# Kernel optimization log

Hardware: AMD Instinct MI355X
Metric: run time of the kernel (lower is better)

Reference implementation:

```python
import jax, jax.numpy as jnp
import numpy as np

B, C, H, W = 16, 512, 32, 32
GROUPS = 8
EPS = 1e-5


def setup_inputs() -> dict:
    key = jax.random.key(0)
    ks = jax.random.split(key, 7)
    s = 1.0 / np.sqrt(C)
    return {
        "x": jax.random.normal(ks[0], (B, C, H, W), dtype=jnp.float32),
        "gamma": jnp.ones((C,), dtype=jnp.float32),
        "beta": jnp.zeros((C,), dtype=jnp.float32),
        "w_qkv": jax.random.normal(ks[1], (3 * C, C), dtype=jnp.float32) * s,
        "b_qkv": jnp.zeros((3 * C,), dtype=jnp.float32),
        "w_proj": jax.random.normal(ks[2], (C, C), dtype=jnp.float32) * s,
        "b_proj": jnp.zeros((C,), dtype=jnp.float32),
    }


def group_norm(x, gamma, beta):
    b, c, h, w = x.shape
    xg = x.reshape(b, GROUPS, c // GROUPS, h, w)
    mean = xg.mean(axis=(2, 3, 4), keepdims=True)
    var = xg.var(axis=(2, 3, 4), keepdims=True)
    xn = ((xg - mean) * jax.lax.rsqrt(var + EPS)).reshape(b, c, h, w)
    return xn * gamma[None, :, None, None] + beta[None, :, None, None]


def reference(x, gamma, beta, w_qkv, b_qkv, w_proj, b_proj):
    b, c, h, w = x.shape
    n = h * w
    hn = group_norm(x, gamma, beta)
    # 1x1 conv == channel matmul: [3C, C] x [B, C, N] -> [B, 3C, N]
    qkv = jnp.einsum('oc,bcn->bon', w_qkv, hn.reshape(b, c, n)) + b_qkv[None, :, None]
    q, k, v = jnp.split(qkv, 3, axis=1)  # each [B, C, N]
    scale = c ** (-0.5)
    # scores [B, N, N]: q^T k
    attn = jax.nn.softmax(jnp.einsum('bcn,bcm->bnm', q, k) * scale, axis=-1)
    out = jnp.einsum('bnm,bcm->bcn', attn, v)  # [B, C, N]
    proj = jnp.einsum('oc,bcn->bon', w_proj, out) + b_proj[None, :, None]
    return x + proj.reshape(b, c, h, w)
```

## Files before the change

### kernel.cpp

```cpp
#include <hip/hip_runtime.h>


#define BATCH 16
#define CCH 512
#define NSP 1024
#define EPSV 1e-5f
#define BK 32
#define HT 4096

typedef short bf16x8 __attribute__((ext_vector_type(8)));
typedef float f32x4 __attribute__((ext_vector_type(4)));

__device__ __forceinline__ unsigned short f2bf(float f) {
    unsigned int u = __float_as_uint(f);
    u += 0x7FFF + ((u >> 16) & 1);
    return (unsigned short)(u >> 16);
}

__device__ __forceinline__ void glds16(const void* g, void* l) {
    __builtin_amdgcn_global_load_lds(
        (const __attribute__((address_space(1))) unsigned int*)g,
        (__attribute__((address_space(3))) unsigned int*)l, 16, 0, 0);
}

#define XCD_MAP(GX_LOG2, PER, xv, yv, bv)                 \
    const int lin_ = blockIdx.x;                          \
    const int xcd_ = lin_ & 7;                            \
    int slot_ = lin_ >> 3;                                \
    const int hi_ = (slot_ >= (PER)) ? 1 : 0;             \
    const int bv = xcd_ + 8 * hi_;                        \
    slot_ -= hi_ * (PER);                                 \
    const int xv = slot_ & ((1 << (GX_LOG2)) - 1);        \
    const int yv = slot_ >> (GX_LOG2);

__device__ __forceinline__ void gemm128_loop(
    const unsigned short* __restrict__ Ag, const unsigned short* __restrict__ Bg,
    int astr, int bstr, int ktot, short* Al, short* Bl, f32x4* acc) {
    const int t = threadIdx.x;
    const int w = t >> 6, lane = t & 63;
    const int wr = (w >> 1) * 64, wc = (w & 1) * 64;
    const int fr = lane & 15, fko = (lane >> 4) * 8;
    const int r0 = t >> 2;
    const int kc = (t & 3) * 8;
    const unsigned short* Ap0 = Ag + (size_t)r0 * astr + kc;
    const unsigned short* Ap1 = Ag + (size_t)(r0 + 64) * astr + kc;
    const unsigned short* Bp0 = Bg + (size_t)r0 * bstr + kc;
    const unsigned short* Bp1 = Bg + (size_t)(r0 + 64) * bstr + kc;
    short* Alw = Al + w * 512;
    short* Blw = Bl + w * 512;
    for (int k0 = 0; k0 < ktot; k0 += 64) {
        glds16(Ap0 + k0, Alw);
        glds16(Ap1 + k0, Alw + 2048);
        glds16(Ap0 + k0 + 32, Alw + HT);
        glds16(Ap1 + k0 + 32, Alw + HT + 2048);
        glds16(Bp0 + k0, Blw);
        glds16(Bp1 + k0, Blw + 2048);
        glds16(Bp0 + k0 + 32, Blw + HT);
        glds16(Bp1 + k0 + 32, Blw + HT + 2048);
        __syncthreads();
#pragma unroll
        for (int h = 0; h < 2; h++) {
            const short* Ab = Al + h * HT;
            const short* Bb = Bl + h * HT;
            bf16x8 af[4], bfr[4];
#pragma unroll
            for (int mi = 0; mi < 4; mi++)
                af[mi] = *(const bf16x8*)(Ab + (wr + mi * 16 + fr) * BK + fko);
#pragma unroll
            for (int ni = 0; ni < 4; ni++)
                bfr[ni] = *(const bf16x8*)(Bb + (wc + ni * 16 + fr) * BK + fko);
#pragma unroll
            for (int mi = 0; mi < 4; mi++)
#pragma unroll
                for (int ni = 0; ni < 4; ni++)
                    acc[mi * 4 + ni] = __builtin_amdgcn_mfma_f32_16x16x32_bf16(
                        af[mi], bfr[ni], acc[mi * 4 + ni], 0, 0, 0);
        }
        __syncthreads();
    }
}

#define EPI_SETUP()                                          \
    const int t = threadIdx.x, lane = t & 63, w = t >> 6;    \
    const int wr = (w >> 1) * 64, wc = (w & 1) * 64;         \
    const int fr = lane & 15, rr0 = (lane >> 4) * 4;

#define ACC_INIT(acc)                                        \
    f32x4 acc[16];                                           \
    _Pragma("unroll") for (int i = 0; i < 16; i++)           \
        acc[i] = (f32x4){0.f, 0.f, 0.f, 0.f};

__global__ __launch_bounds__(256) void setup_k(
    const float* __restrict__ x, float* __restrict__ stats,
    const float* __restrict__ wa, unsigned short* __restrict__ oa, int na4,
    const float* __restrict__ wb, unsigned short* __restrict__ ob, int nb4,
    float* __restrict__ Lsum) {
    const int t = threadIdx.x;
    if (blockIdx.x < 128) {
        const int bg = blockIdx.x;
        const float4* xp = (const float4*)(x + (size_t)bg * 65536);
        float s = 0.f, q = 0.f;
#pragma unroll
        for (int i = 0; i < 64; i++) {
            float4 v = xp[t + i * 256];
            s += v.x + v.y + v.z + v.w;
            q += v.x * v.x + v.y * v.y + v.z * v.z + v.w * v.w;
        }
#pragma unroll
        for (int off = 32; off; off >>= 1) {
            s += __shfl_down(s, off);
            q += __shfl_down(q, off);
        }
        __shared__ float rs[4], rq[4];
        const int wave = t >> 6, lane = t & 63;
        if (lane == 0) { rs[wave] = s; rq[wave] = q; }
        __syncthreads();
        if (t == 0) {
            float S = rs[0] + rs[1] + rs[2] + rs[3];
            float Q = rq[0] + rq[1] + rq[2] + rq[3];
            const float inv = 1.f / 65536.f;
            float mean = S * inv;
            float var = Q * inv - mean * mean;
            stats[bg * 2] = mean;
            stats[bg * 2 + 1] = rsqrtf(var + EPSV);
        }
    } else if (blockIdx.x < 1152) {
        int i = (blockIdx.x - 128) * 256 + t;
        const float* src;
        unsigned short* dst;
        int j;
        if (i < na4) { src = wa; dst = oa; j = i; }
        else { j = i - na4; if (j >= nb4) return; src = wb; dst = ob; }
        float4 v = ((const float4*)src)[j];
        ushort4 o;
        o.x = f2bf(v.x); o.y = f2bf(v.y); o.z = f2bf(v.z); o.w = f2bf(v.w);
        ((ushort4*)dst)[j] = o;
    } else {
        int i = (blockIdx.x - 1152) * 256 + t;
        ((float4*)Lsum)[i] = (float4){0.f, 0.f, 0.f, 0.f};
    }
}

__global__ __launch_bounds__(256) void gn_tr_k(
    const float* __restrict__ x, const float* __restrict__ gamma,
    const float* __restrict__ beta, const float* __restrict__ stats,
    unsigned short* __restrict__ hn_t) {
    const int nt = blockIdx.x, ct = blockIdx.y, b = blockIdx.z;
    __shared__ __align__(16) unsigned short T[64 * 72];
    const int t = threadIdx.x;
    const float mean = stats[(b * 8 + ct) * 2];
    const float rstd = stats[(b * 8 + ct) * 2 + 1];
    const int cl = t >> 2, nc = t & 3;
    const int c = ct * 64 + cl;
    const float ga = gamma[c] * rstd;
    const float be = beta[c] - mean * ga;
    const float4* xp = (const float4*)(x + ((size_t)b * CCH + c) * NSP + nt * 64);
#pragma unroll
    for (int j = 0; j < 4; j++) {
        float4 v = xp[nc * 4 + j];
        int n = nc * 16 + j * 4;
        T[(n + 0) * 72 + cl] = f2bf(v.x * ga + be);
        T[(n + 1) * 72 + cl] = f2bf(v.y * ga + be);
        T[(n + 2) * 72 + cl] = f2bf(v.z * ga + be);
        T[(n + 3) * 72 + cl] = f2bf(v.w * ga + be);
    }
    __syncthreads();
    const int nl = t >> 2, cc = t & 3;
    unsigned short* dst = hn_t + ((size_t)b * NSP + nt * 64 + nl) * CCH + ct * 64 + cc * 16;
    const unsigned short* src = T + nl * 72 + cc * 16;
    *(uint4*)dst = *(const uint4*)src;
    *(uint4*)(dst + 8) = *(const uint4*)(src + 8);
}

__global__ __launch_bounds__(256) void gemm_qkv_k(
    const unsigned short* __restrict__ hn_t, const unsigned short* __restrict__ wq,
    const float* __restrict__ bq, unsigned short* __restrict__ QKt,
    unsigned short* __restrict__ Vb) {
    __shared__ __align__(16) short Al[2 * HT], Bl[2 * HT];
    XCD_MAP(3, 96, xb, y, b);
    const int ntc = xb * 128;
    ACC_INIT(acc);
    if (y < 8) {
        const int mt = y * 128;
        gemm128_loop(hn_t + ((size_t)b * NSP + mt) * CCH,
                     wq + (size_t)ntc * CCH, CCH, CCH, CCH, Al, Bl, acc);
        unsigned short* Ob = QKt + (size_t)b * NSP * 1024;
        EPI_SETUP();
#pragma unroll
        for (int ni = 0; ni < 4; ni++) {
            int col = ntc + wc + ni * 16 + fr;
            float bias = bq[col];
#pragma unroll
            for (int mi = 0; mi < 4; mi++) {
                int row = mt + wr + mi * 16 + rr0;
#pragma unroll
                for (int r = 0; r < 4; r++)
                    Ob[(size_t)(row + r) * 1024 + col] = f2bf(acc[mi * 4 + ni][r] + bias);
            }
        }
    } else {
        const int mt = (y - 8) * 128;
        gemm128_loop(wq + (size_t)(1024 + mt) * CCH,
                     hn_t + ((size_t)b * NSP + ntc) * CCH, CCH, CCH, CCH, Al, Bl, acc);
        unsigned short* Ob = Vb + (size_t)b * CCH * NSP;
        EPI_SETUP();
#pragma unroll
        for (int mi = 0; mi < 4; mi++) {
            int row = mt + wr + mi * 16 + rr0;
#pragma unroll
            for (int r = 0; r < 4; r++) {
                float bias = bq[1024 + row + r];
#pragma unroll
                for (int ni = 0; ni < 4; ni++) {
                    int col = ntc + wc + ni * 16 + fr;
                    Ob[(size_t)(row + r) * NSP + col] = f2bf(acc[mi * 4 + ni][r] + bias);
                }
            }
        }
    }
}

__global__ __launch_bounds__(256) void gemm_scores_k(
    const unsigned short* __restrict__ QKt, unsigned short* __restrict__ expS,
    float* __restrict__ Lsum) {
    __shared__ __align__(16) short Al[2 * HT], Bl[2 * HT];
    XCD_MAP(3, 64, xb, yb, b);
    const int nt = xb * 128, mt = yb * 128;
    const unsigned short* base = QKt + (size_t)b * NSP * 1024;
    ACC_INIT(acc);
    gemm128_loop(base + (size_t)mt * 1024, base + (size_t)nt * 1024 + 512,
                 1024, 1024, 512, Al, Bl, acc);
    unsigned short* Ob = expS + (size_t)b * NSP * NSP;
    float* Ls = Lsum + (size_t)b * NSP;
    const float scale = 0.044194173824159216f;
    EPI_SETUP();
#pragma unroll
    for (int mi = 0; mi < 4; mi++) {
#pragma unroll
        for (int r = 0; r < 4; r++) {
            const int row = mt + wr + mi * 16 + rr0 + r;
            float rs = 0.f;
#pragma unroll
            for (int ni = 0; ni < 4; ni++) {
                int col = nt + wc + ni * 16 + fr;
                float e = __expf(acc[mi * 4 + ni][r] * scale);
                Ob[(size_t)row * NSP + col] = f2bf(e);
                rs += e;
            }
            rs += __shfl_xor(rs, 1);
            rs += __shfl_xor(rs, 2);
            rs += __shfl_xor(rs, 4);
            rs += __shfl_xor(rs, 8);
            if (fr == 0) atomicAdd(&Ls[row], rs);
        }
    }
}

__global__ __launch_bounds__(256) void gemm_pv_k(
    const unsigned short* __restrict__ expS, const unsigned short* __restrict__ Vb,
    const float* __restrict__ Lsum, unsigned short* __restrict__ At) {
    __shared__ __align__(16) short Al[2 * HT], Bl[2 * HT];
    XCD_MAP(2, 32, xb, yb, b);
    const int ntc = xb * 128, mt = yb * 128;
    ACC_INIT(acc);
    gemm128_loop(expS + ((size_t)b * NSP + mt) * NSP,
                 Vb + ((size_t)b * CCH + ntc) * NSP, NSP, NSP, NSP, Al, Bl, acc);
    unsigned short* Ob = At + (size_t)b * NSP * CCH;
    const float* Ls = Lsum + (size_t)b * NSP;
    EPI_SETUP();
#pragma unroll
    for (int mi = 0; mi < 4; mi++) {
        int row = mt + wr + mi * 16 + rr0;
#pragma unroll
        for (int r = 0; r < 4; r++) {
            float inv = __builtin_amdgcn_rcpf(Ls[row + r]);
#pragma unroll
            for (int ni = 0; ni < 4; ni++) {
                int col = ntc + wc + ni * 16 + fr;
                Ob[(size_t)(row + r) * CCH + col] = f2bf(acc[mi * 4 + ni][r] * inv);
            }
        }
    }
}

__global__ __launch_bounds__(256) void gemm_proj_k(
    const unsigned short* __restrict__ At, const unsigned short* __restrict__ wp,
    const float* __restrict__ bp, const float* __restrict__ x,
    float* __restrict__ out) {
    __shared__ __align__(16) short Al[2 * HT], Bl[2 * HT];
    XCD_MAP(3, 32, xb, yb, b);
    const int nt = xb * 128, mt = yb * 128;
    ACC_INIT(acc);
    gemm128_loop(wp + (size_t)mt * CCH, At + ((size_t)b * NSP + nt) * CCH,
                 CCH, CCH, CCH, Al, Bl, acc);
    const size_t bbase = (size_t)b * CCH * NSP;
    EPI_SETUP();
#pragma unroll
    for (int mi = 0; mi < 4; mi++) {
        int row = mt + wr + mi * 16 + rr0;
#pragma unroll
        for (int r = 0; r < 4; r++) {
            float bias = bp[row + r];
#pragma unroll
            for (int ni = 0; ni < 4; ni++) {
                int col = nt + wc + ni * 16 + fr;
                size_t idx = bbase + (size_t)(row + r) * NSP + col;
                out[idx] = x[idx] + bias + acc[mi * 4 + ni][r];
            }
        }
    }
}

extern "C" void kernel_launch(void* const* d_in, const int* in_sizes, int n_in,
                              void* d_out, int out_size, void* d_ws, size_t ws_size,
                              hipStream_t stream) {
    const float* x = (const float*)d_in[0];
    const float* gamma = (const float*)d_in[1];
    const float* beta = (const float*)d_in[2];
    const float* w_qkv = (const float*)d_in[3];
    const float* b_qkv = (const float*)d_in[4];
    const float* w_proj = (const float*)d_in[5];
    const float* b_proj = (const float*)d_in[6];
    float* out = (float*)d_out;

    char* ws = (char*)d_ws;
    const size_t MB = 1048576;
    unsigned short* wqkv_bf = (unsigned short*)ws;
    unsigned short* wproj_bf = (unsigned short*)(ws + 1572864);
    float* stats = (float*)(ws + 2 * MB);
    float* Lsum = (float*)(ws + 2 * MB + 65536);
    unsigned short* hn_t = (unsigned short*)(ws + 4 * MB);
    unsigned short* At = hn_t;
    unsigned short* QKt = (unsigned short*)(ws + 24 * MB);
    unsigned short* Vb = (unsigned short*)(ws + 60 * MB);
    unsigned short* expS = (unsigned short*)(ws + 80 * MB);

    setup_k<<<1168, 256, 0, stream>>>(x, stats, w_qkv, wqkv_bf, 196608,
                                      w_proj, wproj_bf, 65536, Lsum);
    gn_tr_k<<<dim3(16, 8, BATCH), 256, 0, stream>>>(x, gamma, beta, stats, hn_t);
    gemm_qkv_k<<<1536, 256, 0, stream>>>(hn_t, wqkv_bf, b_qkv, QKt, Vb);
    gemm_scores_k<<<1024, 256, 0, stream>>>(QKt, expS, Lsum);
    gemm_pv_k<<<512, 256, 0, stream>>>(expS, Vb, Lsum, At);
    gemm_proj_k<<<512, 256, 0, stream>>>(At, wproj_bf, b_proj, x, out);
}
```

Before: 209.9 us.

## Replace 128x128 GEMM core with 256x256 8-wave double-buffered pipelined kernel

Swaps the 128x128 tile, 4-wave GEMM loop for a 256x256 tile, 8-wave loop. It double-buffers LDS at 128 KB, uses XOR-swizzled LDS layouts, and interleaves global->LDS staging with MFMA quadrants, using explicit waitcnt, barriers and setprio. All four GEMM kernels are relaunched with 512 threads and a quarter of the blocks. The aim is more data reuse per block, fewer LDS bank conflicts and overlap of memory traffic with matrix math. In exchange there are far fewer blocks (128 for the pv and proj GEMMs on 256 CUs), higher register pressure from 32 accumulators, and the 128 KB of LDS probably limits a CU to one block.

```diff
diff --git a/kernel.cpp b/kernel.cpp
--- a/kernel.cpp
+++ b/kernel.cpp
@@ -5,8 +5,6 @@
 #define CCH 512
 #define NSP 1024
 #define EPSV 1e-5f
-#define BK 32
-#define HT 4096
 
 typedef short bf16x8 __attribute__((ext_vector_type(8)));
 typedef float f32x4 __attribute__((ext_vector_type(4)));
@@ -23,72 +21,110 @@
         (__attribute__((address_space(3))) unsigned int*)l, 16, 0, 0);
 }
 
-#define XCD_MAP(GX_LOG2, PER, xv, yv, bv)                 \
-    const int lin_ = blockIdx.x;                          \
-    const int xcd_ = lin_ & 7;                            \
-    int slot_ = lin_ >> 3;                                \
-    const int hi_ = (slot_ >= (PER)) ? 1 : 0;             \
-    const int bv = xcd_ + 8 * hi_;                        \
-    slot_ -= hi_ * (PER);                                 \
-    const int xv = slot_ & ((1 << (GX_LOG2)) - 1);        \
-    const int yv = slot_ >> (GX_LOG2);
-
-__device__ __forceinline__ void gemm128_loop(
+#define MEMF asm volatile("" ::: "memory")
+#define VMW(n) asm volatile("s_waitcnt vmcnt(" #n ")" ::: "memory")
+#define LGKM(n) asm volatile("s_waitcnt lgkmcnt(" #n ")" ::: "memory")
+#define BAR_ACQ do { MEMF; __builtin_amdgcn_s_barrier(); LGKM(0); \
+                     __builtin_amdgcn_s_setprio(1); } while (0)
+#define BAR_REL do { __builtin_amdgcn_s_setprio(0); MEMF; \
+                     __builtin_amdgcn_s_barrier(); } while (0)
+
+#define STG_A(cbuf, h, kk) do { \
+    const unsigned short* p_ = Asrc + (size_t)((h) * 128) * astr + (kk); \
+    glds16(p_, ldsW + (cbuf) * 16384 + (h) * 8192); \
+    glds16(p_ + (size_t)64 * astr, ldsW + (cbuf) * 16384 + (h) * 8192 + 4096); \
+  } while (0)
+#define STG_B(cbuf, h, kk) do { \
+    const unsigned short* p_ = Bsrc + (size_t)((h) * 128) * bstr + (kk); \
+    glds16(p_, ldsW + 32768 + (cbuf) * 16384 + (h) * 8192); \
+    glds16(p_ + (size_t)64 * bstr, ldsW + 32768 + (cbuf) * 16384 + (h) * 8192 + 4096); \
+  } while (0)
+#define LDA4(cbuf, mq) do { \
+    _Pragma("unroll") for (int mi_ = 0; mi_ < 4; mi_++) { \
+      const short* p_ = L + (cbuf) * 16384 + aRd + ((mq) * 4 + mi_) * 1024; \
+      a[mi_][0] = *(const bf16x8*)(p_ + cA0); \
+      a[mi_][1] = *(const bf16x8*)(p_ + cA1); } \
+  } while (0)
+#define LDB2(cbuf, nq, arr) do { \
+    _Pragma("unroll") for (int ni_ = 0; ni_ < 2; ni_++) { \
+      const short* p_ = L + (cbuf) * 16384 + bRd + ((nq) * 2 + ni_) * 1024; \
+      arr[ni_][0] = *(const bf16x8*)(p_ + cA0); \
+      arr[ni_][1] = *(const bf16x8*)(p_ + cA1); } \
+  } while (0)
+#define MMAQ(mq, nq, arr) do { \
+    _Pragma("unroll") for (int mi_ = 0; mi_ < 4; mi_++) \
+    _Pragma("unroll") for (int ni_ = 0; ni_ < 2; ni_++) { \
+      const int ix_ = ((mq) * 4 + mi_) * 4 + (nq) * 2 + ni_; \
+      acc[ix_] = __builtin_amdgcn_mfma_f32_16x16x32_bf16(a[mi_][0], arr[ni_][0], acc[ix_], 0, 0, 0); \
+      acc[ix_] = __builtin_amdgcn_mfma_f32_16x16x32_bf16(a[mi_][1], arr[ni_][1], acc[ix_], 0, 0, 0); } \
+  } while (0)
+
+__device__ __forceinline__ void gemm256_loop(
     const unsigned short* __restrict__ Ag, const unsigned short* __restrict__ Bg,
-    int astr, int bstr, int ktot, short* Al, short* Bl, f32x4* acc) {
+    int astr, int bstr, int ktot, short* L, f32x4* acc) {
     const int t = threadIdx.x;
-    const int w = t >> 6, lane = t & 63;
-    const int wr = (w >> 1) * 64, wc = (w & 1) * 64;
-    const int fr = lane & 15, fko = (lane >> 4) * 8;
-    const int r0 = t >> 2;
-    const int kc = (t & 3) * 8;
-    const unsigned short* Ap0 = Ag + (size_t)r0 * astr + kc;
-    const unsigned short* Ap1 = Ag + (size_t)(r0 + 64) * astr + kc;
-    const unsigned short* Bp0 = Bg + (size_t)r0 * bstr + kc;
-    const unsigned short* Bp1 = Bg + (size_t)(r0 + 64) * bstr + kc;
-    short* Alw = Al + w * 512;
-    short* Blw = Bl + w * 512;
-    for (int k0 = 0; k0 < ktot; k0 += 64) {
-        glds16(Ap0 + k0, Alw);
-        glds16(Ap1 + k0, Alw + 2048);
-        glds16(Ap0 + k0 + 32, Alw + HT);
-        glds16(Ap1 + k0 + 32, Alw + HT + 2048);
-        glds16(Bp0 + k0, Blw);
-        glds16(Bp1 + k0, Blw + 2048);
-        glds16(Bp0 + k0 + 32, Blw + HT);
-        glds16(Bp1 + k0 + 32, Blw + HT + 2048);
-        __syncthreads();
-#pragma unroll
-        for (int h = 0; h < 2; h++) {
-            const short* Ab = Al + h * HT;
-            const short* Bb = Bl + h * HT;
-            bf16x8 af[4], bfr[4];
-#pragma unroll
-            for (int mi = 0; mi < 4; mi++)
-                af[mi] = *(const bf16x8*)(Ab + (wr + mi * 16 + fr) * BK + fko);
-#pragma unroll
-            for (int ni = 0; ni < 4; ni++)
-                bfr[ni] = *(const bf16x8*)(Bb + (wc + ni * 16 + fr) * BK + fko);
-#pragma unroll
-            for (int mi = 0; mi < 4; mi++)
-#pragma unroll
-                for (int ni = 0; ni < 4; ni++)
-                    acc[mi * 4 + ni] = __builtin_amdgcn_mfma_f32_16x16x32_bf16(
-                        af[mi], bfr[ni], acc[mi * 4 + ni], 0, 0, 0);
-        }
-        __syncthreads();
-    }
-}
-
-#define EPI_SETUP()                                          \
-    const int t = threadIdx.x, lane = t & 63, w = t >> 6;    \
-    const int wr = (w >> 1) * 64, wc = (w & 1) * 64;         \
+    const int lane = t & 63, w = t >> 6;
+    const int wm = w >> 2, wn = w & 3;
+    const int fr = lane & 15, fj = lane >> 4;
+    const int rA = t >> 3;
+    const int jx = ((t & 7) ^ (rA & 7)) * 8;
+    const unsigned short* Asrc = Ag + (size_t)rA * astr + jx;
+    const unsigned short* Bsrc = Bg + (size_t)rA * bstr + jx;
+    short* ldsW = L + w * 512;
+    const int aRd = wm * 8192 + fr * 64;
+    const int bRd = 32768 + (wn >> 1) * 8192 + (wn & 1) * 4096 + fr * 64;
+    const int cA0 = (fj ^ (fr & 7)) * 8;
+    const int cA1 = ((4 + fj) ^ (fr & 7)) * 8;
+    bf16x8 a[4][2], b01[2][2], b23[2][2];
+
+    STG_A(0, 0, 0); STG_A(0, 1, 0); STG_B(0, 0, 0); STG_B(0, 1, 0);
+    STG_B(1, 0, 64); STG_B(1, 1, 64);
+    VMW(4);
+    MEMF; __builtin_amdgcn_s_barrier();
+
+    for (int k0 = 0; k0 < ktot; k0 += 128) {
+        const int kB1 = k0 + 64;
+        const int kN1 = (k0 + 128 < ktot) ? k0 + 128 : 0;
+        const int kN2 = (k0 + 192 < ktot) ? k0 + 192 : 0;
+        LDA4(0, 0); LDB2(0, 0, b01);
+        STG_A(1, 0, kB1);
+        LGKM(8);
+        BAR_ACQ; MMAQ(0, 0, b01); BAR_REL;
+        LDB2(0, 1, b23);
+        STG_A(1, 1, kB1);
+        BAR_ACQ; MMAQ(0, 1, b23); BAR_REL;
+        LDA4(0, 1);
+        STG_B(0, 0, kN1);
+        BAR_ACQ; MMAQ(1, 0, b01); BAR_REL;
+        STG_B(0, 1, kN1);
+        VMW(4);
+        BAR_ACQ; MMAQ(1, 1, b23); BAR_REL;
+        LDA4(1, 0); LDB2(1, 0, b01);
+        STG_A(0, 0, kN1);
+        LGKM(8);
+        BAR_ACQ; MMAQ(0, 0, b01); BAR_REL;
+        LDB2(1, 1, b23);
+        STG_A(0, 1, kN1);
+        BAR_ACQ; MMAQ(0, 1, b23); BAR_REL;
+        LDA4(1, 1);
+        STG_B(1, 0, kN2);
+        BAR_ACQ; MMAQ(1, 0, b01); BAR_REL;
+        STG_B(1, 1, kN2);
+        VMW(4);
+        BAR_ACQ; MMAQ(1, 1, b23); BAR_REL;
+    }
+    VMW(0);
+}
+
+#define ACC_INIT32(acc)                                      \
+    f32x4 acc[32];                                           \
+    _Pragma("unroll") for (int i = 0; i < 32; i++)           \
+        acc[i] = (f32x4){0.f, 0.f, 0.f, 0.f};
+
+#define EPI256()                                             \
+    const int t = threadIdx.x, lane = t & 63, w8 = t >> 6;   \
+    const int wr = (w8 >> 2) * 128, wc = (w8 & 3) * 64;      \
     const int fr = lane & 15, rr0 = (lane >> 4) * 4;
-
-#define ACC_INIT(acc)                                        \
-    f32x4 acc[16];                                           \
-    _Pragma("unroll") for (int i = 0; i < 16; i++)           \
-        acc[i] = (f32x4){0.f, 0.f, 0.f, 0.f};
 
 __global__ __launch_bounds__(256) void setup_k(
     const float* __restrict__ x, float* __restrict__ stats,
@@ -172,47 +208,51 @@
     *(uint4*)(dst + 8) = *(const uint4*)(src + 8);
 }
 
-__global__ __launch_bounds__(256) void gemm_qkv_k(
+__global__ __launch_bounds__(512, 2) void gemm_qkv_k(
     const unsigned short* __restrict__ hn_t, const unsigned short* __restrict__ wq,
     const float* __restrict__ bq, unsigned short* __restrict__ QKt,
     unsigned short* __restrict__ Vb) {
-    __shared__ __align__(16) short Al[2 * HT], Bl[2 * HT];
-    XCD_MAP(3, 96, xb, y, b);
-    const int ntc = xb * 128;
-    ACC_INIT(acc);
-    if (y < 8) {
-        const int mt = y * 128;
-        gemm128_loop(hn_t + ((size_t)b * NSP + mt) * CCH,
-                     wq + (size_t)ntc * CCH, CCH, CCH, CCH, Al, Bl, acc);
+    __shared__ __align__(16) short L[65536];
+    const int lin = blockIdx.x, xcd = lin & 7;
+    int slot = lin >> 3;
+    const int hi = (slot >= 24) ? 1 : 0;
+    const int b = xcd + 8 * hi;
+    slot -= hi * 24;
+    ACC_INIT32(acc);
+    if (slot < 16) {
+        const int mt = (slot & 3) * 256, nt = (slot >> 2) * 256;
+        gemm256_loop(hn_t + ((size_t)b * NSP + mt) * CCH, wq + (size_t)nt * CCH,
+                     CCH, CCH, CCH, L, acc);
         unsigned short* Ob = QKt + (size_t)b * NSP * 1024;
-        EPI_SETUP();
+        EPI256();
 #pragma unroll
         for (int ni = 0; ni < 4; ni++) {
-            int col = ntc + wc + ni * 16 + fr;
-            float bias = bq[col];
-#pragma unroll
-            for (int mi = 0; mi < 4; mi++) {
-                int row = mt + wr + mi * 16 + rr0;
+            const int col = nt + wc + ni * 16 + fr;
+            const float bias = bq[col];
+#pragma unroll
+            for (int mi = 0; mi < 8; mi++) {
+                const int row = mt + wr + mi * 16 + rr0;
 #pragma unroll
                 for (int r = 0; r < 4; r++)
                     Ob[(size_t)(row + r) * 1024 + col] = f2bf(acc[mi * 4 + ni][r] + bias);
             }
         }
     } else {
-        const int mt = (y - 8) * 128;
-        gemm128_loop(wq + (size_t)(1024 + mt) * CCH,
-                     hn_t + ((size_t)b * NSP + ntc) * CCH, CCH, CCH, CCH, Al, Bl, acc);
+        const int s2 = slot - 16;
+        const int mt = (s2 & 1) * 256, nt = (s2 >> 1) * 256;
+        gemm256_loop(wq + (size_t)(1024 + mt) * CCH,
+                     hn_t + ((size_t)b * NSP + nt) * CCH, CCH, CCH, CCH, L, acc);
         unsigned short* Ob = Vb + (size_t)b * CCH * NSP;
-        EPI_SETUP();
-#pragma unroll
-        for (int mi = 0; mi < 4; mi++) {
-            int row = mt + wr + mi * 16 + rr0;
+        EPI256();
+#pragma unroll
+        for (int mi = 0; mi < 8; mi++) {
+            const int row = mt + wr + mi * 16 + rr0;
 #pragma unroll
             for (int r = 0; r < 4; r++) {
-                float bias = bq[1024 + row + r];
+                const float bias = bq[1024 + row + r];
 #pragma unroll
                 for (int ni = 0; ni < 4; ni++) {
-                    int col = ntc + wc + ni * 16 + fr;
+                    const int col = nt + wc + ni * 16 + fr;
                     Ob[(size_t)(row + r) * NSP + col] = f2bf(acc[mi * 4 + ni][r] + bias);
                 }
             }
@@ -220,29 +260,33 @@
     }
 }
 
-__global__ __launch_bounds__(256) void gemm_scores_k(
+__global__ __launch_bounds__(512, 2) void gemm_scores_k(
     const unsigned short* __restrict__ QKt, unsigned short* __restrict__ expS,
     float* __restrict__ Lsum) {
-    __shared__ __align__(16) short Al[2 * HT], Bl[2 * HT];
-    XCD_MAP(3, 64, xb, yb, b);
-    const int nt = xb * 128, mt = yb * 128;
+    __shared__ __align__(16) short L[65536];
+    const int lin = blockIdx.x, xcd = lin & 7;
+    int slot = lin >> 3;
+    const int hi = (slot >= 16) ? 1 : 0;
+    const int b = xcd + 8 * hi;
+    slot -= hi * 16;
+    const int mt = (slot & 3) * 256, nt = (slot >> 2) * 256;
     const unsigned short* base = QKt + (size_t)b * NSP * 1024;
-    ACC_INIT(acc);
-    gemm128_loop(base + (size_t)mt * 1024, base + (size_t)nt * 1024 + 512,
-                 1024, 1024, 512, Al, Bl, acc);
+    ACC_INIT32(acc);
+    gemm256_loop(base + (size_t)mt * 1024, base + (size_t)nt * 1024 + 512,
+                 1024, 1024, 512, L, acc);
     unsigned short* Ob = expS + (size_t)b * NSP * NSP;
     float* Ls = Lsum + (size_t)b * NSP;
     const float scale = 0.044194173824159216f;
-    EPI_SETUP();
-#pragma unroll
-    for (int mi = 0; mi < 4; mi++) {
+    EPI256();
+#pragma unroll
+    for (int mi = 0; mi < 8; mi++) {
 #pragma unroll
         for (int r = 0; r < 4; r++) {
             const int row = mt + wr + mi * 16 + rr0 + r;
             float rs = 0.f;
 #pragma unroll
             for (int ni = 0; ni < 4; ni++) {
-                int col = nt + wc + ni * 16 + fr;
+                const int col = nt + wc + ni * 16 + fr;
                 float e = __expf(acc[mi * 4 + ni][r] * scale);
                 Ob[(size_t)row * NSP + col] = f2bf(e);
                 rs += e;
@@ -256,54 +300,62 @@
     }
 }
 
-__global__ __launch_bounds__(256) void gemm_pv_k(
+__global__ __launch_bounds__(512, 2) void gemm_pv_k(
     const unsigned short* __restrict__ expS, const unsigned short* __restrict__ Vb,
     const float* __restrict__ Lsum, unsigned short* __restrict__ At) {
-    __shared__ __align__(16) short Al[2 * HT], Bl[2 * HT];
-    XCD_MAP(2, 32, xb, yb, b);
-    const int ntc = xb * 128, mt = yb * 128;
-    ACC_INIT(acc);
-    gemm128_loop(expS + ((size_t)b * NSP + mt) * NSP,
-                 Vb + ((size_t)b * CCH + ntc) * NSP, NSP, NSP, NSP, Al, Bl, acc);
+    __shared__ __align__(16) short L[65536];
+    const int lin = blockIdx.x, xcd = lin & 7;
+    int slot = lin >> 3;
+    const int hi = (slot >= 8) ? 1 : 0;
+    const int b = xcd + 8 * hi;
+    slot -= hi * 8;
+    const int nt = (slot & 1) * 256, mt = (slot >> 1) * 256;
+    ACC_INIT32(acc);
+    gemm256_loop(expS + ((size_t)b * NSP + mt) * NSP,
+                 Vb + ((size_t)b * CCH + nt) * NSP, NSP, NSP, NSP, L, acc);
     unsigned short* Ob = At + (size_t)b * NSP * CCH;
     const float* Ls = Lsum + (size_t)b * NSP;
-    EPI_SETUP();
-#pragma unroll
-    for (int mi = 0; mi < 4; mi++) {
-        int row = mt + wr + mi * 16 + rr0;
+    EPI256();
+#pragma unroll
+    for (int mi = 0; mi < 8; mi++) {
+        const int row = mt + wr + mi * 16 + rr0;
 #pragma unroll
         for (int r = 0; r < 4; r++) {
-            float inv = __builtin_amdgcn_rcpf(Ls[row + r]);
+            const float inv = __builtin_amdgcn_rcpf(Ls[row + r]);
 #pragma unroll
             for (int ni = 0; ni < 4; ni++) {
-                int col = ntc + wc + ni * 16 + fr;
+                const int col = nt + wc + ni * 16 + fr;
                 Ob[(size_t)(row + r) * CCH + col] = f2bf(acc[mi * 4 + ni][r] * inv);
             }
         }
     }
 }
 
-__global__ __launch_bounds__(256) void gemm_proj_k(
+__global__ __launch_bounds__(512, 2) void gemm_proj_k(
     const unsigned short* __restrict__ At, const unsigned short* __restrict__ wp,
     const float* __restrict__ bp, const float* __restrict__ x,
     float* __restrict__ out) {
-    __shared__ __align__(16) short Al[2 * HT], Bl[2 * HT];
-    XCD_MAP(3, 32, xb, yb, b);
-    const int nt = xb * 128, mt = yb * 128;
-    ACC_INIT(acc);
-    gemm128_loop(wp + (size_t)mt * CCH, At + ((size_t)b * NSP + nt) * CCH,
-                 CCH, CCH, CCH, Al, Bl, acc);
+    __shared__ __align__(16) short L[65536];
+    const int lin = blockIdx.x, xcd = lin & 7;
+    int slot = lin >> 3;
+    const int hi = (slot >= 8) ? 1 : 0;
+    const int b = xcd + 8 * hi;
+    slot -= hi * 8;
+    const int nt = (slot & 3) * 256, mt = (slot >> 2) * 256;
+    ACC_INIT32(acc);
+    gemm256_loop(wp + (size_t)mt * CCH, At + ((size_t)b * NSP + nt) * CCH,
+                 CCH, CCH, CCH, L, acc);
     const size_t bbase = (size_t)b * CCH * NSP;
-    EPI_SETUP();
-#pragma unroll
-    for (int mi = 0; mi < 4; mi++) {
-        int row = mt + wr + mi * 16 + rr0;
+    EPI256();
+#pragma unroll
+    for (int mi = 0; mi < 8; mi++) {
+        const int row = mt + wr + mi * 16 + rr0;
 #pragma unroll
         for (int r = 0; r < 4; r++) {
-            float bias = bp[row + r];
+            const float bias = bp[row + r];
 #pragma unroll
             for (int ni = 0; ni < 4; ni++) {
-                int col = nt + wc + ni * 16 + fr;
+                const int col = nt + wc + ni * 16 + fr;
                 size_t idx = bbase + (size_t)(row + r) * NSP + col;
                 out[idx] = x[idx] + bias + acc[mi * 4 + ni][r];
             }
@@ -338,8 +390,8 @@
     setup_k<<<1168, 256, 0, stream>>>(x, stats, w_qkv, wqkv_bf, 196608,
                                       w_proj, wproj_bf, 65536, Lsum);
     gn_tr_k<<<dim3(16, 8, BATCH), 256, 0, stream>>>(x, gamma, beta, stats, hn_t);
-    gemm_qkv_k<<<1536, 256, 0, stream>>>(hn_t, wqkv_bf, b_qkv, QKt, Vb);
-    gemm_scores_k<<<1024, 256, 0, stream>>>(QKt, expS, Lsum);
-    gemm_pv_k<<<512, 256, 0, stream>>>(expS, Vb, Lsum, At);
-    gemm_proj_k<<<512, 256, 0, stream>>>(At, wproj_bf, b_proj, x, out);
-}
+    gemm_qkv_k<<<384, 512, 0, stream>>>(hn_t, wqkv_bf, b_qkv, QKt, Vb);
+    gemm_scores_k<<<256, 512, 0, stream>>>(QKt, expS, Lsum);
+    gemm_pv_k<<<128, 512, 0, stream>>>(expS, Vb, Lsum, At);
+    gemm_proj_k<<<128, 512, 0, stream>>>(At, wproj_bf, b_proj, x, out);
+}
```

New measurement: 221.1 us. +5.3%, slower.
